# Optimization experiments

Hardware: AMD Instinct MI355X
Metric: run time of the kernel (lower is better)

Reference implementation:

```python
import jax, jax.numpy as jnp
import numpy as np

D_MODEL = 1024
NUM_HEADS = 16
D_K = D_MODEL // NUM_HEADS
THETA = 10000.0
BATCH = 2
SEQ = 2048


def apply_rope(x, token_positions):
    # x: [B, H, S, D_K]; token_positions: [S] int
    half = D_K // 2
    inv_freq = THETA ** (-(jnp.arange(half, dtype=jnp.float32) * 2.0) / D_K)  # [half]
    angles = token_positions.astype(jnp.float32)[:, None] * inv_freq[None, :]  # [S, half]
    cos = jnp.cos(angles)  # [S, half]
    sin = jnp.sin(angles)
    x1 = x[..., 0::2]  # even indices
    x2 = x[..., 1::2]  # odd indices
    out_even = x1 * cos - x2 * sin
    out_odd = x1 * sin + x2 * cos
    # interleave back: [..., S, half, 2] -> [..., S, D_K]
    return jnp.stack([out_even, out_odd], axis=-1).reshape(x.shape)


def setup_inputs() -> dict:
    key = jax.random.key(0)
    ks = jax.random.split(key, 5)
    x = jax.random.normal(ks[0], (BATCH, SEQ, D_MODEL), dtype=jnp.float32)
    token_positions = jnp.arange(SEQ, dtype=jnp.int64)
    scale = 0.02
    Wq = jax.random.normal(ks[1], (D_MODEL, D_MODEL), dtype=jnp.float32) * scale
    Wk = jax.random.normal(ks[2], (D_MODEL, D_MODEL), dtype=jnp.float32) * scale
    Wv = jax.random.normal(ks[3], (D_MODEL, D_MODEL), dtype=jnp.float32) * scale
    Wo = jax.random.normal(ks[4], (D_MODEL, D_MODEL), dtype=jnp.float32) * scale
    return {"x": x, "token_positions": token_positions, "Wq": Wq, "Wk": Wk, "Wv": Wv, "Wo": Wo}


def reference(x, token_positions, Wq, Wk, Wv, Wo):
    B, S, _ = x.shape
    # cs336 Linear: y = x @ W.T with W of shape (out, in), no bias
    def proj(W):
        h = jnp.einsum('bsd,od->bso', x, W)
        return h.reshape(B, S, NUM_HEADS, D_K).transpose(0, 2, 1, 3)  # [B,H,S,Dk]
    Q = apply_rope(proj(Wq), token_positions)
    K = apply_rope(proj(Wk), token_positions)
    V = proj(Wv)
    scores = jnp.einsum('bhqd,bhkd->bhqk', Q, K) / jnp.sqrt(jnp.float32(D_K))
    causal = jnp.tril(jnp.ones((S, S), dtype=bool))
    scores = jnp.where(causal, scores, -jnp.inf)
    attn = jax.nn.softmax(scores, axis=-1)
    out = jnp.einsum('bhqk,bhkd->bhqd', attn, V)  # [B,H,S,Dk]
    out = out.transpose(0, 2, 1, 3).reshape(B, S, D_MODEL)
    return jnp.einsum('bsd,od->bso', out, Wo)
```

## Files before the change

kernel.cpp:

```cpp
#include <hip/hip_runtime.h>
#include <hip/hip_bf16.h>
#include <math.h>

#define NHEADS 16
#define DKH 64
#define SEQ 2048
#define DMODEL 1024

typedef __attribute__((ext_vector_type(8))) short short8;
typedef __attribute__((ext_vector_type(4))) float f32x4;

__device__ __forceinline__ short f2bf(float f) {
  unsigned u = __float_as_uint(f);
  unsigned r = (u + 0x7fffu + ((u >> 16) & 1u)) >> 16;
  return (short)r;
}

__device__ __forceinline__ short8 pack8(float4 a, float4 b) {
  short8 v;
  v[0] = f2bf(a.x); v[1] = f2bf(a.y); v[2] = f2bf(a.z); v[3] = f2bf(a.w);
  v[4] = f2bf(b.x); v[5] = f2bf(b.y); v[6] = f2bf(b.z); v[7] = f2bf(b.w);
  return v;
}

__device__ __forceinline__ int swz(int r, int gran) {
  return r * 64 + ((gran ^ (r & 7)) << 3);
}

__global__ void rope_table_kernel(const int* __restrict__ tp,
                                  float* __restrict__ ct, float* __restrict__ st) {
  int idx = blockIdx.x * 256 + threadIdx.x;
  if (idx >= SEQ * 32) return;
  int s = idx >> 5, i = idx & 31;
  int is64 = (tp[1] == 0);
  int p = is64 ? tp[2 * s] : tp[s];
  float invf = powf(10000.0f, -(2.0f * (float)i) / 64.0f);
  float a = (float)p * invf;
  ct[idx] = cosf(a);
  st[idx] = sinf(a);
}

__global__ __launch_bounds__(256) void precast_kernel(
    const float* __restrict__ X, const float* __restrict__ Wq,
    const float* __restrict__ Wk, const float* __restrict__ Wv,
    const float* __restrict__ Wo,
    short* __restrict__ Xb, short* __restrict__ Wqb, short* __restrict__ Wkb,
    short* __restrict__ Wvb, short* __restrict__ Wob) {
  int i = blockIdx.x * 256 + threadIdx.x;
  const float* src; short* dst; int off;
  if (i < 524288) { src = X; dst = Xb; off = i; }
  else {
    int k = i - 524288; int w = k >> 17; off = k & 131071;
    src = (w == 0) ? Wq : (w == 1) ? Wk : (w == 2) ? Wv : Wo;
    dst = (w == 0) ? Wqb : (w == 1) ? Wkb : (w == 2) ? Wvb : Wob;
  }
  const float4* p = reinterpret_cast<const float4*>(src) + 2 * (size_t)off;
  float4 a = p[0], b = p[1];
  reinterpret_cast<short8*>(dst)[off] = pack8(a, b);
}

__global__ __launch_bounds__(256) void gemm_qkv_kernel(
    const short* __restrict__ X, const short* __restrict__ Wq,
    const short* __restrict__ Wk, const short* __restrict__ Wv,
    short* __restrict__ Qb, short* __restrict__ Kb, short* __restrict__ Vb,
    const float* __restrict__ ct, const float* __restrict__ st) {
  __shared__ __align__(16) short As[64 * 64];
  __shared__ __align__(16) short Bs[64 * 64];
  const int tm = blockIdx.x;
  const int tn = blockIdx.y;
  const int tid = threadIdx.x;
  const int wave = tid >> 6, lane = tid & 63;
  const int l15 = lane & 15, quad = lane >> 4;

  const int mid = (tn * 64) >> 10;
  const int n0 = (tn * 64) & 1023;
  const short* W = (mid == 0) ? Wq : (mid == 1 ? Wk : Wv);
  const short* Arow = X + (size_t)(tm * 64) * DMODEL;
  const short* Wrow = W + (size_t)n0 * DMODEL;

  f32x4 acc[4];
#pragma unroll
  for (int i = 0; i < 4; i++) acc[i] = (f32x4){0.f, 0.f, 0.f, 0.f};

  for (int kk = 0; kk < DMODEL; kk += 64) {
#pragma unroll
    for (int i = 0; i < 2; i++) {
      int g = tid + i * 256;
      int r = g >> 3, c = g & 7;
      uint4 va = *reinterpret_cast<const uint4*>(Arow + (size_t)r * DMODEL + kk + c * 8);
      *reinterpret_cast<uint4*>(&As[swz(r, c)]) = va;
      uint4 vb = *reinterpret_cast<const uint4*>(Wrow + (size_t)r * DMODEL + kk + c * 8);
      *reinterpret_cast<uint4*>(&Bs[swz(r, c)]) = vb;
    }
    __syncthreads();
    short8 af0, af1;
    {
      int r = wave * 16 + l15;
      af0 = *reinterpret_cast<const short8*>(&As[swz(r, quad)]);
      af1 = *reinterpret_cast<const short8*>(&As[swz(r, 4 + quad)]);
    }
#pragma unroll
    for (int nb = 0; nb < 4; nb++) {
      int r = nb * 16 + l15;
      short8 bf0 = *reinterpret_cast<const short8*>(&Bs[swz(r, quad)]);
      acc[nb] = __builtin_amdgcn_mfma_f32_16x16x32_bf16(af0, bf0, acc[nb], 0, 0, 0);
      short8 bf1 = *reinterpret_cast<const short8*>(&Bs[swz(r, 4 + quad)]);
      acc[nb] = __builtin_amdgcn_mfma_f32_16x16x32_bf16(af1, bf1, acc[nb], 0, 0, 0);
    }
    __syncthreads();
  }
#pragma unroll
  for (int nb = 0; nb < 4; nb++) {
    int nl = n0 + nb * 16 + l15;
    int h = nl >> 6, dd = nl & 63;
#pragma unroll
    for (int reg = 0; reg < 4; reg++) {
      int rg = tm * 64 + wave * 16 + quad * 4 + reg;
      int b = rg >> 11, s = rg & 2047;
      float v = acc[nb][reg];
      size_t oi = (((size_t)(b * NHEADS + h)) * SEQ + s) * DKH + dd;
      if (mid == 2) {
        Vb[oi] = f2bf(v);
      } else {
        float pv = __shfl_xor(v, 1);
        int fi = dd >> 1;
        float c = ct[s * 32 + fi], sn = st[s * 32 + fi];
        float o = (dd & 1) ? (pv * sn + v * c) : (v * c - pv * sn);
        ((mid == 0) ? Qb : Kb)[oi] = f2bf(o);
      }
    }
  }
}

__global__ __launch_bounds__(256, 4) void attn_kernel(
    const short* __restrict__ Qb, const short* __restrict__ Kb,
    const short* __restrict__ Vb, short* __restrict__ Ob) {
  __shared__ __align__(16) short QPs[64 * 64];
  __shared__ __align__(16) short Ks[2][64 * 64];
  __shared__ __align__(16) short Vs[2][64 * 64];

  const int id = blockIdx.x;
  const int xx = id & 7;
  const int mm = (((id >> 3) & 3) + (id >> 8)) & 3;
  const int bh = id >> 5;
  const int qt = (mm == 0) ? (31 - xx) : (mm == 1) ? (16 + xx)
               : (mm == 2) ? (15 - xx) : xx;

  const int tid = threadIdx.x;
  const int wave = tid >> 6, lane = tid & 63;
  const int l15 = lane & 15, quad = lane >> 4;
  const int sr0 = tid >> 3, sc = tid & 7;

  const short* Qp = Qb + (size_t)bh * SEQ * DKH;
  const short* Kp = Kb + (size_t)bh * SEQ * DKH;
  const short* Vp = Vb + (size_t)bh * SEQ * DKH;

  uint4 kreg[2], vreg[2];
#pragma unroll
  for (int i = 0; i < 2; i++) {
    int r = sr0 + i * 32;
    kreg[i] = *reinterpret_cast<const uint4*>(Kp + (size_t)r * DKH + sc * 8);
    vreg[i] = *reinterpret_cast<const uint4*>(Vp + (size_t)r * DKH + sc * 8);
  }
#pragma unroll
  for (int i = 0; i < 2; i++) {
    int r = sr0 + i * 32;
    uint4 v = *reinterpret_cast<const uint4*>(Qp + (size_t)(qt * 64 + r) * DKH + sc * 8);
    *reinterpret_cast<uint4*>(&QPs[swz(r, sc)]) = v;
  }
#pragma unroll
  for (int i = 0; i < 2; i++) {
    int r = sr0 + i * 32;
    *reinterpret_cast<uint4*>(&Ks[0][swz(r, sc)]) = kreg[i];
    const short* vsp = reinterpret_cast<const short*>(&vreg[i]);
#pragma unroll
    for (int j = 0; j < 8; j++) {
      int dv = sc * 8 + j;
      Vs[0][dv * 64 + ((((r >> 3) ^ (dv & 7) ^ (dv >> 3)) & 7) << 3) + (r & 7)] = vsp[j];
    }
  }
  __syncthreads();
  short8 qf0, qf1;
  {
    int r = wave * 16 + l15;
    qf0 = *reinterpret_cast<const short8*>(&QPs[swz(r, quad)]);
    qf1 = *reinterpret_cast<const short8*>(&QPs[swz(r, 4 + quad)]);
  }

  f32x4 accO[4];
#pragma unroll
  for (int i = 0; i < 4; i++) accO[i] = (f32x4){0.f, 0.f, 0.f, 0.f};
  float rs[4] = {0.f, 0.f, 0.f, 0.f};

  const float SCL = 0.125f * 1.44269504089f;
  const float FM = 13.0f;

  int buf = 0;
  for (int kt = 0; kt <= qt; kt++) {
    if (kt < qt) {
#pragma unroll
      for (int i = 0; i < 2; i++) {
        int r = (kt + 1) * 64 + sr0 + i * 32;
        kreg[i] = *reinterpret_cast<const uint4*>(Kp + (size_t)r * DKH + sc * 8);
        vreg[i] = *reinterpret_cast<const uint4*>(Vp + (size_t)r * DKH + sc * 8);
      }
    }

    f32x4 sa[4];
#pragma unroll
    for (int nb = 0; nb < 4; nb++) {
      sa[nb] = (f32x4){0.f, 0.f, 0.f, 0.f};
      int r = nb * 16 + l15;
      short8 kf0 = *reinterpret_cast<const short8*>(&Ks[buf][swz(r, quad)]);
      sa[nb] = __builtin_amdgcn_mfma_f32_16x16x32_bf16(qf0, kf0, sa[nb], 0, 0, 0);
      short8 kf1 = *reinterpret_cast<const short8*>(&Ks[buf][swz(r, 4 + quad)]);
      sa[nb] = __builtin_amdgcn_mfma_f32_16x16x32_bf16(qf1, kf1, sa[nb], 0, 0, 0);
    }

    const bool diag = (kt == qt);
#pragma unroll
    for (int nb = 0; nb < 4; nb++)
#pragma unroll
      for (int reg = 0; reg < 4; reg++) {
        float p = exp2f(sa[nb][reg] * SCL - FM);
        if (diag && (nb * 16 + l15) > (wave * 16 + quad * 4 + reg)) p = 0.f;
        rs[reg] += p;
        int r = quad * 4 + reg, col = nb * 16 + l15;
        QPs[swz(wave * 16 + r, col >> 3) + (col & 7)] = f2bf(p);
      }

    short8 pf0, pf1;
    {
      int r = wave * 16 + l15;
      pf0 = *reinterpret_cast<const short8*>(&QPs[swz(r, quad)]);
      pf1 = *reinterpret_cast<const short8*>(&QPs[swz(r, 4 + quad)]);
    }
#pragma unroll
    for (int db = 0; db < 4; db++) {
      int dv = db * 16 + l15;
      int fsw = (dv & 7) ^ (dv >> 3);
      short8 vf0 = *reinterpret_cast<const short8*>(
          &Vs[buf][dv * 64 + (((quad ^ fsw) & 7) << 3)]);
      accO[db] = __builtin_amdgcn_mfma_f32_16x16x32_bf16(pf0, vf0, accO[db], 0, 0, 0);
      short8 vf1 = *reinterpret_cast<const short8*>(
          &Vs[buf][dv * 64 + ((((quad + 4) ^ fsw) & 7) << 3)]);
      accO[db] = __builtin_amdgcn_mfma_f32_16x16x32_bf16(pf1, vf1, accO[db], 0, 0, 0);
    }

    if (kt < qt) {
      int nbuf = buf ^ 1;
#pragma unroll
      for (int i = 0; i < 2; i++) {
        int r = sr0 + i * 32;
        *reinterpret_cast<uint4*>(&Ks[nbuf][swz(r, sc)]) = kreg[i];
        const short* vsp = reinterpret_cast<const short*>(&vreg[i]);
#pragma unroll
        for (int j = 0; j < 8; j++) {
          int dv = sc * 8 + j;
          Vs[nbuf][dv * 64 + ((((r >> 3) ^ (dv & 7) ^ (dv >> 3)) & 7) << 3) + (r & 7)] = vsp[j];
        }
      }
      __syncthreads();
      buf = nbuf;
    }
  }

  float lrow[4];
#pragma unroll
  for (int reg = 0; reg < 4; reg++) {
    float t = rs[reg];
#pragma unroll
    for (int off = 1; off < 16; off <<= 1) t += __shfl_xor(t, off);
    lrow[reg] = t;
  }

  int b = bh >> 4, h = bh & 15;
#pragma unroll
  for (int db = 0; db < 4; db++)
#pragma unroll
    for (int reg = 0; reg < 4; reg++) {
      int s = qt * 64 + wave * 16 + quad * 4 + reg;
      int dv = db * 16 + l15;
      float o = accO[db][reg] / lrow[reg];
      Ob[((size_t)(b * SEQ + s)) * DMODEL + h * DKH + dv] = f2bf(o);
    }
}

__global__ __launch_bounds__(256) void gemm_out_kernel(
    const short* __restrict__ X, const short* __restrict__ Wo, float* __restrict__ Out) {
  __shared__ __align__(16) short As[64 * 64];
  __shared__ __align__(16) short Bs[64 * 64];
  const int tm = blockIdx.x;
  const int tn = blockIdx.y;
  const int tid = threadIdx.x;
  const int wave = tid >> 6, lane = tid & 63;
  const int l15 = lane & 15, quad = lane >> 4;

  const short* Arow = X + (size_t)(tm * 64) * DMODEL;
  const short* Wrow = Wo + (size_t)(tn * 64) * DMODEL;

  f32x4 acc[4];
#pragma unroll
  for (int i = 0; i < 4; i++) acc[i] = (f32x4){0.f, 0.f, 0.f, 0.f};

  for (int kk = 0; kk < DMODEL; kk += 64) {
#pragma unroll
    for (int i = 0; i < 2; i++) {
      int g = tid + i * 256;
      int r = g >> 3, c = g & 7;
      uint4 va = *reinterpret_cast<const uint4*>(Arow + (size_t)r * DMODEL + kk + c * 8);
      *reinterpret_cast<uint4*>(&As[swz(r, c)]) = va;
      uint4 vb = *reinterpret_cast<const uint4*>(Wrow + (size_t)r * DMODEL + kk + c * 8);
      *reinterpret_cast<uint4*>(&Bs[swz(r, c)]) = vb;
    }
    __syncthreads();
    short8 af0, af1;
    {
      int r = wave * 16 + l15;
      af0 = *reinterpret_cast<const short8*>(&As[swz(r, quad)]);
      af1 = *reinterpret_cast<const short8*>(&As[swz(r, 4 + quad)]);
    }
#pragma unroll
    for (int nb = 0; nb < 4; nb++) {
      int r = nb * 16 + l15;
      short8 bf0 = *reinterpret_cast<const short8*>(&Bs[swz(r, quad)]);
      acc[nb] = __builtin_amdgcn_mfma_f32_16x16x32_bf16(af0, bf0, acc[nb], 0, 0, 0);
      short8 bf1 = *reinterpret_cast<const short8*>(&Bs[swz(r, 4 + quad)]);
      acc[nb] = __builtin_amdgcn_mfma_f32_16x16x32_bf16(af1, bf1, acc[nb], 0, 0, 0);
    }
    __syncthreads();
  }
#pragma unroll
  for (int nb = 0; nb < 4; nb++)
#pragma unroll
    for (int reg = 0; reg < 4; reg++) {
      int rg = tm * 64 + wave * 16 + quad * 4 + reg;
      int col = tn * 64 + nb * 16 + l15;
      Out[(size_t)rg * DMODEL + col] = acc[nb][reg];
    }
}

extern "C" void kernel_launch(void* const* d_in, const int* in_sizes, int n_in,
                              void* d_out, int out_size, void* d_ws, size_t ws_size,
                              hipStream_t stream) {
  (void)in_sizes; (void)n_in; (void)out_size; (void)ws_size;
  const float* X  = (const float*)d_in[0];
  const int*   tp = (const int*)d_in[1];
  const float* Wq = (const float*)d_in[2];
  const float* Wk = (const float*)d_in[3];
  const float* Wv = (const float*)d_in[4];
  const float* Wo = (const float*)d_in[5];
  float* Out = (float*)d_out;

  short* Qb  = (short*)d_ws;
  short* Kb  = Qb + 4194304;
  short* Vb  = Kb + 4194304;
  short* Ab  = Vb + 4194304;
  short* Xb  = Ab + 4194304;
  short* Wqb = Xb + 4194304;
  short* Wkb = Wqb + 1048576;
  short* Wvb = Wkb + 1048576;
  short* Wob = Wvb + 1048576;
  float* ct  = (float*)(Wob + 1048576);
  float* st  = ct + SEQ * 32;

  rope_table_kernel<<<dim3(256), dim3(256), 0, stream>>>(tp, ct, st);
  precast_kernel<<<dim3(4096), dim3(256), 0, stream>>>(X, Wq, Wk, Wv, Wo,
                                                       Xb, Wqb, Wkb, Wvb, Wob);
  gemm_qkv_kernel<<<dim3(64, 48), dim3(256), 0, stream>>>(Xb, Wqb, Wkb, Wvb,
                                                          Qb, Kb, Vb, ct, st);
  attn_kernel<<<dim3(1024), dim3(256), 0, stream>>>(Qb, Kb, Vb, Ab);
  gemm_out_kernel<<<dim3(64, 16), dim3(256), 0, stream>>>(Ab, Wob, Out);
}
```

Measured before the change: 213.1 us.

## Enlarge GEMM tiles and load operands directly into LDS

The QKV projection moves from 64x64 to 128x128 output tiles and the output projection from 64x64 to 128x64, with each wave owning a 64x64 or 64x32 sub-tile. This raises register-level reuse and the MFMA-to-load ratio. Operand staging now uses global_load_lds to copy straight from global memory into LDS, skipping the register round trip, and XOR-swizzles the source address to match the existing LDS layout. The cost is more accumulator registers and fewer blocks, which may lower occupancy and leave CUs idle on the output GEMM, which now launches 512 blocks.

```diff
diff --git a/kernel.cpp b/kernel.cpp
--- a/kernel.cpp
+++ b/kernel.cpp
@@ -9,6 +9,11 @@
 
 typedef __attribute__((ext_vector_type(8))) short short8;
 typedef __attribute__((ext_vector_type(4))) float f32x4;
+
+#define GLDS16(g, l)                                         \
+  __builtin_amdgcn_global_load_lds(                          \
+      (__attribute__((address_space(1))) void*)(void*)(g),   \
+      (__attribute__((address_space(3))) void*)(l), 16, 0, 0)
 
 __device__ __forceinline__ short f2bf(float f) {
   unsigned u = __float_as_uint(f);
@@ -64,72 +69,89 @@
     const short* __restrict__ Wk, const short* __restrict__ Wv,
     short* __restrict__ Qb, short* __restrict__ Kb, short* __restrict__ Vb,
     const float* __restrict__ ct, const float* __restrict__ st) {
-  __shared__ __align__(16) short As[64 * 64];
-  __shared__ __align__(16) short Bs[64 * 64];
+  __shared__ __align__(16) short As[128 * 64];
+  __shared__ __align__(16) short Bs[128 * 64];
   const int tm = blockIdx.x;
   const int tn = blockIdx.y;
   const int tid = threadIdx.x;
   const int wave = tid >> 6, lane = tid & 63;
   const int l15 = lane & 15, quad = lane >> 4;
-
-  const int mid = (tn * 64) >> 10;
-  const int n0 = (tn * 64) & 1023;
+  const int wm = wave >> 1, wn = wave & 1;
+
+  const int mid = tn >> 3;
+  const int n0 = (tn & 7) * 128;
   const short* W = (mid == 0) ? Wq : (mid == 1 ? Wk : Wv);
-  const short* Arow = X + (size_t)(tm * 64) * DMODEL;
-  const short* Wrow = W + (size_t)n0 * DMODEL;
-
-  f32x4 acc[4];
-#pragma unroll
-  for (int i = 0; i < 4; i++) acc[i] = (f32x4){0.f, 0.f, 0.f, 0.f};
-
-  for (int kk = 0; kk < DMODEL; kk += 64) {
-#pragma unroll
-    for (int i = 0; i < 2; i++) {
-      int g = tid + i * 256;
-      int r = g >> 3, c = g & 7;
-      uint4 va = *reinterpret_cast<const uint4*>(Arow + (size_t)r * DMODEL + kk + c * 8);
-      *reinterpret_cast<uint4*>(&As[swz(r, c)]) = va;
-      uint4 vb = *reinterpret_cast<const uint4*>(Wrow + (size_t)r * DMODEL + kk + c * 8);
-      *reinterpret_cast<uint4*>(&Bs[swz(r, c)]) = vb;
+  const short* Abase = X + (size_t)(tm * 128) * DMODEL;
+  const short* Bbase = W + (size_t)n0 * DMODEL;
+
+  const int lr = lane >> 3;
+  const int lc = (lane & 7) ^ lr;
+
+  f32x4 acc[4][4];
+#pragma unroll
+  for (int mb = 0; mb < 4; mb++)
+#pragma unroll
+    for (int nb = 0; nb < 4; nb++) acc[mb][nb] = (f32x4){0.f, 0.f, 0.f, 0.f};
+
+  for (int kk = 0; kk < 16; kk++) {
+    const short* Ak = Abase + kk * 64;
+    const short* Bk = Bbase + kk * 64;
+#pragma unroll
+    for (int i = 0; i < 4; i++) {
+      int R = i * 32 + wave * 8;
+      GLDS16(Ak + (size_t)(R + lr) * DMODEL + lc * 8, &As[R * 64 + lane * 8]);
+    }
+#pragma unroll
+    for (int i = 0; i < 4; i++) {
+      int R = i * 32 + wave * 8;
+      GLDS16(Bk + (size_t)(R + lr) * DMODEL + lc * 8, &Bs[R * 64 + lane * 8]);
     }
     __syncthreads();
-    short8 af0, af1;
-    {
-      int r = wave * 16 + l15;
-      af0 = *reinterpret_cast<const short8*>(&As[swz(r, quad)]);
-      af1 = *reinterpret_cast<const short8*>(&As[swz(r, 4 + quad)]);
-    }
+#pragma unroll
+    for (int kg = 0; kg < 2; kg++) {
+      short8 af[4], bf[4];
+#pragma unroll
+      for (int mb = 0; mb < 4; mb++) {
+        int r = wm * 64 + mb * 16 + l15;
+        af[mb] = *reinterpret_cast<const short8*>(&As[swz(r, kg * 4 + quad)]);
+      }
+#pragma unroll
+      for (int nb = 0; nb < 4; nb++) {
+        int r = wn * 64 + nb * 16 + l15;
+        bf[nb] = *reinterpret_cast<const short8*>(&Bs[swz(r, kg * 4 + quad)]);
+      }
+#pragma unroll
+      for (int mb = 0; mb < 4; mb++)
+#pragma unroll
+        for (int nb = 0; nb < 4; nb++)
+          acc[mb][nb] = __builtin_amdgcn_mfma_f32_16x16x32_bf16(af[mb], bf[nb], acc[mb][nb], 0, 0, 0);
+    }
+    __syncthreads();
+  }
+
+#pragma unroll
+  for (int mb = 0; mb < 4; mb++)
 #pragma unroll
     for (int nb = 0; nb < 4; nb++) {
-      int r = nb * 16 + l15;
-      short8 bf0 = *reinterpret_cast<const short8*>(&Bs[swz(r, quad)]);
-      acc[nb] = __builtin_amdgcn_mfma_f32_16x16x32_bf16(af0, bf0, acc[nb], 0, 0, 0);
-      short8 bf1 = *reinterpret_cast<const short8*>(&Bs[swz(r, 4 + quad)]);
-      acc[nb] = __builtin_amdgcn_mfma_f32_16x16x32_bf16(af1, bf1, acc[nb], 0, 0, 0);
-    }
-    __syncthreads();
-  }
-#pragma unroll
-  for (int nb = 0; nb < 4; nb++) {
-    int nl = n0 + nb * 16 + l15;
-    int h = nl >> 6, dd = nl & 63;
-#pragma unroll
-    for (int reg = 0; reg < 4; reg++) {
-      int rg = tm * 64 + wave * 16 + quad * 4 + reg;
-      int b = rg >> 11, s = rg & 2047;
-      float v = acc[nb][reg];
-      size_t oi = (((size_t)(b * NHEADS + h)) * SEQ + s) * DKH + dd;
-      if (mid == 2) {
-        Vb[oi] = f2bf(v);
-      } else {
-        float pv = __shfl_xor(v, 1);
-        int fi = dd >> 1;
-        float c = ct[s * 32 + fi], sn = st[s * 32 + fi];
-        float o = (dd & 1) ? (pv * sn + v * c) : (v * c - pv * sn);
-        ((mid == 0) ? Qb : Kb)[oi] = f2bf(o);
-      }
-    }
-  }
+      int nl = n0 + wn * 64 + nb * 16 + l15;
+      int h = nl >> 6, dd = nl & 63;
+#pragma unroll
+      for (int reg = 0; reg < 4; reg++) {
+        int rg = tm * 128 + wm * 64 + mb * 16 + quad * 4 + reg;
+        int b = rg >> 11, s = rg & 2047;
+        float v = acc[mb][nb][reg];
+        size_t oi = (((size_t)(b * NHEADS + h)) * SEQ + s) * DKH + dd;
+        if (mid == 2) {
+          Vb[oi] = f2bf(v);
+        } else {
+          float pv = __shfl_xor(v, 1);
+          int fi = dd >> 1;
+          float c = ct[s * 32 + fi], sn = st[s * 32 + fi];
+          float o = (dd & 1) ? (pv * sn + v * c) : (v * c - pv * sn);
+          ((mid == 0) ? Qb : Kb)[oi] = f2bf(o);
+        }
+      }
+    }
 }
 
 __global__ __launch_bounds__(256, 4) void attn_kernel(
@@ -288,56 +310,72 @@
 
 __global__ __launch_bounds__(256) void gemm_out_kernel(
     const short* __restrict__ X, const short* __restrict__ Wo, float* __restrict__ Out) {
-  __shared__ __align__(16) short As[64 * 64];
+  __shared__ __align__(16) short As[128 * 64];
   __shared__ __align__(16) short Bs[64 * 64];
   const int tm = blockIdx.x;
   const int tn = blockIdx.y;
   const int tid = threadIdx.x;
   const int wave = tid >> 6, lane = tid & 63;
   const int l15 = lane & 15, quad = lane >> 4;
-
-  const short* Arow = X + (size_t)(tm * 64) * DMODEL;
-  const short* Wrow = Wo + (size_t)(tn * 64) * DMODEL;
-
-  f32x4 acc[4];
-#pragma unroll
-  for (int i = 0; i < 4; i++) acc[i] = (f32x4){0.f, 0.f, 0.f, 0.f};
-
-  for (int kk = 0; kk < DMODEL; kk += 64) {
+  const int wm = wave >> 1, wn = wave & 1;
+
+  const short* Abase = X + (size_t)(tm * 128) * DMODEL;
+  const short* Bbase = Wo + (size_t)(tn * 64) * DMODEL;
+
+  const int lr = lane >> 3;
+  const int lc = (lane & 7) ^ lr;
+
+  f32x4 acc[4][2];
+#pragma unroll
+  for (int mb = 0; mb < 4; mb++)
+#pragma unroll
+    for (int nb = 0; nb < 2; nb++) acc[mb][nb] = (f32x4){0.f, 0.f, 0.f, 0.f};
+
+  for (int kk = 0; kk < 16; kk++) {
+    const short* Ak = Abase + kk * 64;
+    const short* Bk = Bbase + kk * 64;
+#pragma unroll
+    for (int i = 0; i < 4; i++) {
+      int R = i * 32 + wave * 8;
+      GLDS16(Ak + (size_t)(R + lr) * DMODEL + lc * 8, &As[R * 64 + lane * 8]);
+    }
 #pragma unroll
     for (int i = 0; i < 2; i++) {
-      int g = tid + i * 256;
-      int r = g >> 3, c = g & 7;
-      uint4 va = *reinterpret_cast<const uint4*>(Arow + (size_t)r * DMODEL + kk + c * 8);
-      *reinterpret_cast<uint4*>(&As[swz(r, c)]) = va;
-      uint4 vb = *reinterpret_cast<const uint4*>(Wrow + (size_t)r * DMODEL + kk + c * 8);
-      *reinterpret_cast<uint4*>(&Bs[swz(r, c)]) = vb;
+      int R = i * 32 + wave * 8;
+      GLDS16(Bk + (size_t)(R + lr) * DMODEL + lc * 8, &Bs[R * 64 + lane * 8]);
     }
     __syncthreads();
-    short8 af0, af1;
-    {
-      int r = wave * 16 + l15;
-      af0 = *reinterpret_cast<const short8*>(&As[swz(r, quad)]);
-      af1 = *reinterpret_cast<const short8*>(&As[swz(r, 4 + quad)]);
-    }
-#pragma unroll
-    for (int nb = 0; nb < 4; nb++) {
-      int r = nb * 16 + l15;
-      short8 bf0 = *reinterpret_cast<const short8*>(&Bs[swz(r, quad)]);
-      acc[nb] = __builtin_amdgcn_mfma_f32_16x16x32_bf16(af0, bf0, acc[nb], 0, 0, 0);
-      short8 bf1 = *reinterpret_cast<const short8*>(&Bs[swz(r, 4 + quad)]);
-      acc[nb] = __builtin_amdgcn_mfma_f32_16x16x32_bf16(af1, bf1, acc[nb], 0, 0, 0);
+#pragma unroll
+    for (int kg = 0; kg < 2; kg++) {
+      short8 af[4], bf[2];
+#pragma unroll
+      for (int mb = 0; mb < 4; mb++) {
+        int r = wm * 64 + mb * 16 + l15;
+        af[mb] = *reinterpret_cast<const short8*>(&As[swz(r, kg * 4 + quad)]);
+      }
+#pragma unroll
+      for (int nb = 0; nb < 2; nb++) {
+        int r = wn * 32 + nb * 16 + l15;
+        bf[nb] = *reinterpret_cast<const short8*>(&Bs[swz(r, kg * 4 + quad)]);
+      }
+#pragma unroll
+      for (int mb = 0; mb < 4; mb++)
+#pragma unroll
+        for (int nb = 0; nb < 2; nb++)
+          acc[mb][nb] = __builtin_amdgcn_mfma_f32_16x16x32_bf16(af[mb], bf[nb], acc[mb][nb], 0, 0, 0);
     }
     __syncthreads();
   }
 #pragma unroll
-  for (int nb = 0; nb < 4; nb++)
-#pragma unroll
-    for (int reg = 0; reg < 4; reg++) {
-      int rg = tm * 64 + wave * 16 + quad * 4 + reg;
-      int col = tn * 64 + nb * 16 + l15;
-      Out[(size_t)rg * DMODEL + col] = acc[nb][reg];
-    }
+  for (int mb = 0; mb < 4; mb++)
+#pragma unroll
+    for (int nb = 0; nb < 2; nb++)
+#pragma unroll
+      for (int reg = 0; reg < 4; reg++) {
+        int rg = tm * 128 + wm * 64 + mb * 16 + quad * 4 + reg;
+        int col = tn * 64 + wn * 32 + nb * 16 + l15;
+        Out[(size_t)rg * DMODEL + col] = acc[mb][nb][reg];
+      }
 }
 
 extern "C" void kernel_launch(void* const* d_in, const int* in_sizes, int n_in,
@@ -367,8 +405,8 @@
   rope_table_kernel<<<dim3(256), dim3(256), 0, stream>>>(tp, ct, st);
   precast_kernel<<<dim3(4096), dim3(256), 0, stream>>>(X, Wq, Wk, Wv, Wo,
                                                        Xb, Wqb, Wkb, Wvb, Wob);
-  gemm_qkv_kernel<<<dim3(64, 48), dim3(256), 0, stream>>>(Xb, Wqb, Wkb, Wvb,
+  gemm_qkv_kernel<<<dim3(32, 24), dim3(256), 0, stream>>>(Xb, Wqb, Wkb, Wvb,
                                                           Qb, Kb, Vb, ct, st);
   attn_kernel<<<dim3(1024), dim3(256), 0, stream>>>(Qb, Kb, Vb, Ab);
-  gemm_out_kernel<<<dim3(64, 16), dim3(256), 0, stream>>>(Ab, Wob, Out);
-}
+  gemm_out_kernel<<<dim3(32, 16), dim3(256), 0, stream>>>(Ab, Wob, Out);
+}
```

After: 217.9 us. 1.02x slower.
